# Optimization experiments

Measured on AMD Instinct MI355X. Metric: run time of the kernel, lower is better.

The kernel has to match this reference:

```python
import jax, jax.numpy as jnp
import numpy as np

V, Tb, D, H, L = 50257, 1024, 768, 12, 12
HS = D // H  # head size 64
DF = 4 * D   # MLP hidden 3072


def setup_inputs() -> dict:
    key = jax.random.key(0)
    ks = jax.random.split(key, 24)
    s = 0.02
    inp = {}
    inp['x'] = jax.random.randint(ks[0], (1, Tb), 0, V, dtype=jnp.int64)
    inp['wte'] = jax.random.normal(ks[1], (V, D), jnp.float32) * s
    inp['wpe'] = jax.random.normal(ks[2], (Tb, D), jnp.float32) * s
    # per-layer, per-head QKV linears, stacked: [L, H, D, HS]
    inp['Wq'] = jax.random.normal(ks[3], (L, H, D, HS), jnp.float32) * s
    inp['bq'] = jnp.zeros((L, H, HS), jnp.float32)
    inp['Wk'] = jax.random.normal(ks[4], (L, H, D, HS), jnp.float32) * s
    inp['bk'] = jnp.zeros((L, H, HS), jnp.float32)
    inp['Wv'] = jax.random.normal(ks[5], (L, H, D, HS), jnp.float32) * s
    inp['bv'] = jnp.zeros((L, H, HS), jnp.float32)
    inp['ln1_s'] = jnp.ones((L, D), jnp.float32)
    inp['ln1_b'] = jnp.zeros((L, D), jnp.float32)
    inp['W1'] = jax.random.normal(ks[6], (L, D, DF), jnp.float32) * s
    inp['b1'] = jnp.zeros((L, DF), jnp.float32)
    inp['W2'] = jax.random.normal(ks[7], (L, DF, D), jnp.float32) * s
    inp['b2'] = jnp.zeros((L, D), jnp.float32)
    inp['ln2_s'] = jnp.ones((L, D), jnp.float32)
    inp['ln2_b'] = jnp.zeros((L, D), jnp.float32)
    inp['lnf_s'] = jnp.ones((D,), jnp.float32)
    inp['lnf_b'] = jnp.zeros((D,), jnp.float32)
    inp['Wlm'] = jax.random.normal(ks[8], (D, V), jnp.float32) * s
    return inp


def _layernorm(x, scale, bias, eps=1e-5):
    mu = jnp.mean(x, axis=-1, keepdims=True)
    var = jnp.var(x, axis=-1, keepdims=True)
    return (x - mu) * jax.lax.rsqrt(var + eps) * scale + bias


def _gpt2_forward(x, wte, wpe, Wq, bq, Wk, bk, Wv, bv, ln1_s, ln1_b,
                  W1, b1, W2, b2, ln2_s, ln2_b, lnf_s, lnf_b, Wlm):
    B, T = x.shape
    h = wte[x] + wpe[jnp.arange(T)][None]  # [B, T, D]
    mask = jnp.tril(jnp.ones((T, T), jnp.bool_))
    for l in range(L):
        xn = _layernorm(h, ln1_s[l], ln1_b[l])
        # per-head linears, stacked -> [B, H, T, HS]
        q = jnp.einsum('btd,hde->bhte', xn, Wq[l]) + bq[l][None, :, None, :]
        k = jnp.einsum('btd,hde->bhte', xn, Wk[l]) + bk[l][None, :, None, :]
        v = jnp.einsum('btd,hde->bhte', xn, Wv[l]) + bv[l][None, :, None, :]
        # NOTE: original module does NOT scale scores by 1/sqrt(head_size)
        scores = jnp.einsum('bhte,bhse->bhts', q, k)
        scores = jnp.where(mask[None, None], scores, -jnp.inf)
        w = jax.nn.softmax(scores, axis=-1)
        attn = jnp.einsum('bhts,bhse->bhte', w, v)
        attn = attn.transpose(0, 2, 1, 3).reshape(B, T, H * HS)
        h = h + attn  # residual (no output projection in original)
        xn2 = _layernorm(h, ln2_s[l], ln2_b[l])
        mlp = jnp.einsum('btd,df->btf', xn2, W1[l]) + b1[l]
        mlp = jax.nn.gelu(mlp, approximate=False)  # nn.GELU default = exact
        mlp = jnp.einsum('btf,fd->btd', mlp, W2[l]) + b2[l]
        h = h + mlp
    h = _layernorm(h, lnf_s, lnf_b)
    logits = jnp.einsum('btd,dv->btv', h, Wlm)  # lm_head, no bias
    return logits


def reference(x, wte, wpe, Wq, bq, Wk, bk, Wv, bv, ln1_s, ln1_b,
              W1, b1, W2, b2, ln2_s, ln2_b, lnf_s, lnf_b, Wlm):
    return _gpt2_forward(x, wte, wpe, Wq, bq, Wk, bk, Wv, bv, ln1_s, ln1_b,
                         W1, b1, W2, b2, ln2_s, ln2_b, lnf_s, lnf_b, Wlm)
```

## Files before the change

### kernel.cpp

```cpp
#include <hip/hip_runtime.h>
#include <math.h>

#define TLEN 1024
#define DM   768
#define NH   12
#define HSZ  64
#define DF_  3072
#define NL   12
#define VC   50257
#define VCP  50304
#define NPAN (VCP/128)

typedef __attribute__((ext_vector_type(8))) short bf16x8;
typedef __attribute__((ext_vector_type(4))) float f32x4;

__device__ __forceinline__ float gelu_exact(float x){
  return 0.5f * x * (1.0f + erff(x * 0.70710678118654752f));
}
__device__ __forceinline__ short f2bf(float f){
  union { float f; unsigned u; } x; x.f = f;
  unsigned r = x.u + 0x7fffu + ((x.u >> 16) & 1u);
  return (short)(r >> 16);
}
__device__ __forceinline__ void gl16(const void* g, void* l){
  __builtin_amdgcn_global_load_lds(
      (const __attribute__((address_space(1))) unsigned int*)g,
      (__attribute__((address_space(3))) unsigned int*)l, 16, 0, 0);
}

__global__ __launch_bounds__(256) void embed_k(const int* __restrict__ x,
    const float* __restrict__ wte, const float* __restrict__ wpe,
    float* __restrict__ h)
{
  int i = blockIdx.x * 256 + threadIdx.x;
  int t = i / DM, d = i - t * DM;
  h[i] = wte[(size_t)x[t] * DM + d] + wpe[i];
}

__global__ __launch_bounds__(256) void ln_k(const float* __restrict__ in,
    const float* __restrict__ sc, const float* __restrict__ bi,
    short* __restrict__ out)
{
  int w = threadIdx.x >> 6, lane = threadIdx.x & 63;
  int row = blockIdx.x * 4 + w;
  const float* r = in + (size_t)row * DM;
  float v[12];
  float s = 0.f, s2 = 0.f;
  #pragma unroll
  for (int i = 0; i < 12; i++){
    float xv = r[lane + i * 64];
    v[i] = xv; s += xv; s2 += xv * xv;
  }
  #pragma unroll
  for (int off = 32; off; off >>= 1){
    s  += __shfl_xor(s,  off);
    s2 += __shfl_xor(s2, off);
  }
  float mu  = s * (1.0f / DM);
  float var = s2 * (1.0f / DM) - mu * mu;
  float rs  = rsqrtf(var + 1e-5f);
  short* o = out + (size_t)row * DM;
  #pragma unroll
  for (int i = 0; i < 12; i++){
    int c = lane + i * 64;
    o[c] = f2bf((v[i] - mu) * rs * sc[c] + bi[c]);
  }
}

__global__ __launch_bounds__(256) void tc_k(const float* __restrict__ in,
    short* __restrict__ out, int K, int N, int ntiles, int per_mat,
    size_t in_stride, size_t out_stride)
{
  __shared__ short sh[64][65];
  int b = blockIdx.x;
  int l = b / per_mat, r = b - l * per_mat;
  int nt = r % ntiles, kt = r / ntiles;
  const float* ip = in + (size_t)l * in_stride;
  short* op = out + (size_t)l * out_stride;
  int n0 = nt * 64, k0 = kt * 64;
  int tid = threadIdx.x;
  if ((N & 3) == 0){
    #pragma unroll
    for (int it = 0; it < 4; it++){
      int idx = it * 256 + tid;
      int k = idx >> 4, n4 = (idx & 15) * 4;
      float4 v = *(const float4*)(ip + (size_t)(k0 + k) * N + n0 + n4);
      sh[k][n4+0] = f2bf(v.x); sh[k][n4+1] = f2bf(v.y);
      sh[k][n4+2] = f2bf(v.z); sh[k][n4+3] = f2bf(v.w);
    }
  } else {
    #pragma unroll
    for (int it = 0; it < 16; it++){
      int idx = it * 256 + tid;
      int k = idx >> 6, n = idx & 63;
      float v = (n0 + n < N) ? ip[(size_t)(k0 + k) * N + n0 + n] : 0.f;
      sh[k][n] = f2bf(v);
    }
  }
  __syncthreads();
  #pragma unroll
  for (int it = 0; it < 2; it++){
    int n = it * 32 + (tid >> 3);
    int kc = (tid & 7) * 8;
    bf16x8 v;
    #pragma unroll
    for (int u = 0; u < 8; u++) v[u] = sh[kc + u][n];
    *(bf16x8*)(op + (size_t)(n0 + n) * K + k0 + kc) = v;
  }
}

__global__ __launch_bounds__(256) void tcqkv_k(const float* __restrict__ Wq,
    const float* __restrict__ Wk, const float* __restrict__ Wv,
    short* __restrict__ out)
{
  __shared__ short sh[64][65];
  int b = blockIdx.x;
  int l = b / 144; int r = b - l * 144;
  int h = r / 12, kt = r - h * 12;
  int tid = threadIdx.x;
  for (int p = 0; p < 3; p++){
    const float* ip = (p == 0 ? Wq : p == 1 ? Wk : Wv)
                      + ((size_t)(l * NH + h) * DM + kt * 64) * 64;
    if (p) __syncthreads();
    #pragma unroll
    for (int it = 0; it < 4; it++){
      int idx = it * 256 + tid;
      int k = idx >> 4, e4 = (idx & 15) * 4;
      float4 v = *(const float4*)(ip + (size_t)k * 64 + e4);
      sh[k][e4+0] = f2bf(v.x); sh[k][e4+1] = f2bf(v.y);
      sh[k][e4+2] = f2bf(v.z); sh[k][e4+3] = f2bf(v.w);
    }
    __syncthreads();
    short* op = out + (size_t)l * 2304 * DM + (size_t)(p * DM + h * 64) * DM;
    #pragma unroll
    for (int it = 0; it < 2; it++){
      int e = it * 32 + (tid >> 3);
      int kc = (tid & 7) * 8;
      bf16x8 v;
      #pragma unroll
      for (int u = 0; u < 8; u++) v[u] = sh[kc + u][e];
      *(bf16x8*)(op + (size_t)e * DM + kt * 64 + kc) = v;
    }
  }
}

template<int MODE, int FI, int FJ>
__global__ __launch_bounds__(256) void mg_k(
    const short* __restrict__ A, const short* __restrict__ Bt,
    const float* __restrict__ b0, const float* __restrict__ b1,
    const float* __restrict__ b2,
    void* __restrict__ C0, void* __restrict__ C1, void* __restrict__ C2)
{
  constexpr int LDA    = (MODE == 2) ? DF_ : DM;
  constexpr int BM     = FI * 32;
  constexpr int BN     = FJ * 32;
  constexpr int ABYTES = BM * 64 * 2;
  constexpr int BBYTES = BN * 64 * 2;
  __shared__ __align__(16) char lds[2 * (ABYTES + BBYTES)];

  int tid = threadIdx.x;
  int wid = tid >> 6, lane = tid & 63;
  int l15 = lane & 15, l4 = lane >> 4;
  int wr = wid >> 1, wc = wid & 1;

  int m0, n0;
  if (MODE == 3){
    int xcd = blockIdx.x & 7, slot = blockIdx.x >> 3;
    int nb = xcd + 8 * (slot >> 3);
    if (nb >= NPAN) return;
    m0 = (slot & 7) * BM;
    n0 = nb * BN;
  } else {
    m0 = blockIdx.x * BM;
    n0 = blockIdx.y * BN;
  }
  int kbeg = (MODE == 2) ? blockIdx.z * (DF_ / 4) : 0;
  int nk   = ((MODE == 2) ? DF_ / 4 : LDA) / 64;

  f32x4 acc[FI][FJ] = {};
  int wbase = (tid & ~63) * 16;

  auto stage = [&](int k0, int b){
    char* ab = lds + b * ABYTES;
    char* bb = lds + 2 * ABYTES + b * BBYTES;
    #pragma unroll
    for (int ia = 0; ia < FI; ia++){
      int d = ia * 256 + tid;
      int row = d >> 3, gs = (d & 7) ^ (row & 7);
      gl16(A + (size_t)(m0 + row) * LDA + k0 + gs * 8, ab + ia * 4096 + wbase);
    }
    #pragma unroll
    for (int ib = 0; ib < FJ; ib++){
      int d = ib * 256 + tid;
      int row = d >> 3, gs = (d & 7) ^ (row & 7);
      gl16(Bt + (size_t)(n0 + row) * LDA + k0 + gs * 8, bb + ib * 4096 + wbase);
    }
  };

  stage(kbeg, 0);
  int cur = 0;
  for (int t = 0; t < nk; ++t){
    int k0 = kbeg + t * 64;
    if (t + 1 < nk){
      stage(k0 + 64, cur ^ 1);
      if constexpr (FI + FJ == 4) asm volatile("s_waitcnt vmcnt(4)" ::: "memory");
      else                        asm volatile("s_waitcnt vmcnt(8)" ::: "memory");
    } else {
      asm volatile("s_waitcnt vmcnt(0)" ::: "memory");
    }
    __builtin_amdgcn_s_barrier();
    __builtin_amdgcn_sched_barrier(0);

    char* ab = lds + cur * ABYTES;
    char* bb = lds + 2 * ABYTES + cur * BBYTES;
    #pragma unroll
    for (int kk = 0; kk < 2; kk++){
      bf16x8 af[FI], bfr[FJ];
      #pragma unroll
      for (int i = 0; i < FI; i++){
        int row = wr * (FI * 16) + i * 16 + l15;
        af[i] = *(const bf16x8*)(ab + row * 128 + (((kk * 4 + l4) ^ (row & 7)) * 16));
      }
      #pragma unroll
      for (int j = 0; j < FJ; j++){
        int row = wc * (FJ * 16) + j * 16 + l15;
        bfr[j] = *(const bf16x8*)(bb + row * 128 + (((kk * 4 + l4) ^ (row & 7)) * 16));
      }
      #pragma unroll
      for (int i = 0; i < FI; i++)
        #pragma unroll
        for (int j = 0; j < FJ; j++)
          acc[i][j] = __builtin_amdgcn_mfma_f32_16x16x32_bf16(af[i], bfr[j], acc[i][j], 0, 0, 0);
    }
    __builtin_amdgcn_sched_barrier(0);
    __builtin_amdgcn_s_barrier();
    cur ^= 1;
  }

  #pragma unroll
  for (int i = 0; i < FI; i++){
    int rowb = m0 + wr * (FI * 16) + i * 16 + l4 * 4;
    #pragma unroll
    for (int j = 0; j < FJ; j++){
      int col = n0 + wc * (FJ * 16) + j * 16 + l15;
      if (MODE == 0){
        int p = col / DM, within = col - p * DM;
        const float* bp = (p == 0) ? b0 : (p == 1) ? b1 : b2;
        float bb2 = bp[within];
        int hd = within >> 6, e = within & 63;
        if (p < 2){
          short* dst = (short*)((p == 0) ? C0 : C1);
          #pragma unroll
          for (int r = 0; r < 4; r++)
            dst[((size_t)hd * TLEN + rowb + r) * 64 + e] = f2bf(acc[i][j][r] + bb2);
        } else {
          short4 pk;
          pk.x = f2bf(acc[i][j][0] + bb2); pk.y = f2bf(acc[i][j][1] + bb2);
          pk.z = f2bf(acc[i][j][2] + bb2); pk.w = f2bf(acc[i][j][3] + bb2);
          *(short4*)((short*)C2 + ((size_t)hd * 64 + e) * TLEN + rowb) = pk;
        }
      } else if (MODE == 1){
        #pragma unroll
        for (int r = 0; r < 4; r++)
          ((short*)C0)[(size_t)(rowb + r) * DF_ + col] =
              f2bf(gelu_exact(acc[i][j][r] + b0[col]));
      } else if (MODE == 2){
        #pragma unroll
        for (int r = 0; r < 4; r++){
          float add = acc[i][j][r] + (blockIdx.z == 0 ? b0[col] : 0.f);
          atomicAdd((float*)C0 + (size_t)(rowb + r) * DM + col, add);
        }
      } else {
        if (col < VC){
          #pragma unroll
          for (int r = 0; r < 4; r++)
            ((float*)C0)[(size_t)(rowb + r) * VC + col] = acc[i][j][r];
        }
      }
    }
  }
}

__global__ __launch_bounds__(256) void attn_k(const short* __restrict__ q,
    const short* __restrict__ k, const short* __restrict__ vt,
    float* __restrict__ h)
{
  __shared__ short P_lds[4][16][72];
  int tid = threadIdx.x;
  int wid = tid >> 6, lane = tid & 63;
  int l15 = lane & 15, l4 = lane >> 4;
  int head = blockIdx.x >> 4, qt = blockIdx.x & 15;
  int qb = qt * 64 + wid * 16;

  const short* qh = q  + (size_t)head * TLEN * 64;
  const short* kh = k  + (size_t)head * TLEN * 64;
  const short* vh = vt + (size_t)head * 64 * TLEN;

  bf16x8 qf[2];
  qf[0] = *(const bf16x8*)(qh + (size_t)(qb + l15) * 64 + l4 * 8);
  qf[1] = *(const bf16x8*)(qh + (size_t)(qb + l15) * 64 + 32 + l4 * 8);

  f32x4 O[4] = {};
  float mrow[4] = {-3e38f, -3e38f, -3e38f, -3e38f};
  float lrow[4] = {0.f, 0.f, 0.f, 0.f};

  for (int kv0 = 0; kv0 <= qb + 15; kv0 += 64){
    f32x4 S[4] = {};
    #pragma unroll
    for (int kk = 0; kk < 2; kk++){
      #pragma unroll
      for (int j = 0; j < 4; j++){
        bf16x8 kf = *(const bf16x8*)(kh + (size_t)(kv0 + j*16 + l15) * 64
                                     + kk*32 + l4*8);
        S[j] = __builtin_amdgcn_mfma_f32_16x16x32_bf16(qf[kk], kf, S[j], 0, 0, 0);
      }
    }
    if (kv0 + 63 > qb){
      #pragma unroll
      for (int j = 0; j < 4; j++){
        int kvc = kv0 + j*16 + l15;
        #pragma unroll
        for (int r = 0; r < 4; r++)
          if (kvc > qb + l4*4 + r) S[j][r] = -3e38f;
      }
    }
    #pragma unroll
    for (int r = 0; r < 4; r++){
      float mx = fmaxf(fmaxf(S[0][r], S[1][r]), fmaxf(S[2][r], S[3][r]));
      #pragma unroll
      for (int off = 1; off < 16; off <<= 1) mx = fmaxf(mx, __shfl_xor(mx, off));
      float mn = fmaxf(mrow[r], mx);
      float corr = __expf(mrow[r] - mn);
      mrow[r] = mn;
      float sm = 0.f;
      #pragma unroll
      for (int j = 0; j < 4; j++){
        float p = __expf(S[j][r] - mn);
        S[j][r] = p; sm += p;
      }
      #pragma unroll
      for (int off = 1; off < 16; off <<= 1) sm += __shfl_xor(sm, off);
      lrow[r] = lrow[r] * corr + sm;
      #pragma unroll
      for (int j = 0; j < 4; j++) O[j][r] *= corr;
    }
    #pragma unroll
    for (int j = 0; j < 4; j++)
      #pragma unroll
      for (int r = 0; r < 4; r++)
        P_lds[wid][l4*4 + r][j*16 + l15] = f2bf(S[j][r]);
    #pragma unroll
    for (int kk = 0; kk < 2; kk++){
      bf16x8 pa = *(const bf16x8*)(&P_lds[wid][l15][kk*32 + l4*8]);
      #pragma unroll
      for (int jd = 0; jd < 4; jd++){
        bf16x8 vf = *(const bf16x8*)(vh + (size_t)(jd*16 + l15) * TLEN
                                     + kv0 + kk*32 + l4*8);
        O[jd] = __builtin_amdgcn_mfma_f32_16x16x32_bf16(pa, vf, O[jd], 0, 0, 0);
      }
    }
  }

  #pragma unroll
  for (int r = 0; r < 4; r++){
    float inv = 1.0f / lrow[r];
    int t = qb + l4*4 + r;
    #pragma unroll
    for (int jd = 0; jd < 4; jd++){
      int d = head * 64 + jd*16 + l15;
      h[(size_t)t * DM + d] += O[jd][r] * inv;
    }
  }
}

extern "C" void kernel_launch(void* const* d_in, const int* in_sizes, int n_in,
                              void* d_out, int out_size, void* d_ws, size_t ws_size,
                              hipStream_t stream)
{
  const int*   x    = (const int*)  d_in[0];
  const float* wte  = (const float*)d_in[1];
  const float* wpe  = (const float*)d_in[2];
  const float* Wq   = (const float*)d_in[3];
  const float* bq   = (const float*)d_in[4];
  const float* Wk   = (const float*)d_in[5];
  const float* bk   = (const float*)d_in[6];
  const float* Wv   = (const float*)d_in[7];
  const float* bv   = (const float*)d_in[8];
  const float* ln1s = (const float*)d_in[9];
  const float* ln1b = (const float*)d_in[10];
  const float* W1   = (const float*)d_in[11];
  const float* b1   = (const float*)d_in[12];
  const float* W2   = (const float*)d_in[13];
  const float* b2   = (const float*)d_in[14];
  const float* ln2s = (const float*)d_in[15];
  const float* ln2b = (const float*)d_in[16];
  const float* lnfs = (const float*)d_in[17];
  const float* lnfb = (const float*)d_in[18];
  const float* Wlm  = (const float*)d_in[19];
  float* out = (float*)d_out;

  const size_t SZ_QKVT = (size_t)NL * 2304 * DM * 2;
  const size_t SZ_W1T  = (size_t)NL * DF_ * DM * 2;
  const size_t SZ_W2T  = (size_t)NL * DM * DF_ * 2;
  const size_t SZ_WLMT = (size_t)VCP * DM * 2;
  const size_t SZ_H    = (size_t)TLEN * DM * 4;
  const size_t SZ_BF   = (size_t)TLEN * DM * 2;

  char* ws = (char*)d_ws;
  short* wqkvT = (short*)ws;  ws += SZ_QKVT;
  short* w1T   = (short*)ws;  ws += SZ_W1T;
  short* w2T   = (short*)ws;  ws += SZ_W2T;
  short* wlmT  = (short*)ws;  ws += SZ_WLMT;
  float* h     = (float*)ws;  ws += SZ_H;
  short* qb    = (short*)ws;  ws += SZ_BF;
  short* kb    = (short*)ws;  ws += SZ_BF;
  short* vtb   = (short*)ws;  ws += SZ_BF;
  short* xnb   = (short*)ws;  ws += SZ_BF;
  short* mhb   = (short*)ws;

  tcqkv_k<<<NL*NH*12, 256, 0, stream>>>(Wq, Wk, Wv, wqkvT);
  tc_k<<<NL*48*12, 256, 0, stream>>>(W1, w1T, DM, DF_, 48, 576,
                                     (size_t)DM*DF_, (size_t)DM*DF_);
  tc_k<<<NL*12*48, 256, 0, stream>>>(W2, w2T, DF_, DM, 12, 576,
                                     (size_t)DM*DF_, (size_t)DM*DF_);
  tc_k<<<786*12, 256, 0, stream>>>(Wlm, wlmT, DM, VC, 786, 786*12, 0, 0);

  embed_k<<<TLEN*DM/256, 256, 0, stream>>>(x, wte, wpe, h);

  for (int l = 0; l < NL; ++l){
    ln_k<<<TLEN/4, 256, 0, stream>>>(h, ln1s + l*DM, ln1b + l*DM, xnb);
    mg_k<0,2,2><<<dim3(16,36), 256, 0, stream>>>(xnb, wqkvT + (size_t)l*2304*DM,
        bq + l*DM, bk + l*DM, bv + l*DM, qb, kb, vtb);
    attn_k<<<NH*16, 256, 0, stream>>>(qb, kb, vtb, h);
    ln_k<<<TLEN/4, 256, 0, stream>>>(h, ln2s + l*DM, ln2b + l*DM, xnb);
    mg_k<1,2,2><<<dim3(16,48), 256, 0, stream>>>(xnb, w1T + (size_t)l*DF_*DM,
        b1 + l*DF_, nullptr, nullptr, mhb, nullptr, nullptr);
    mg_k<2,2,2><<<dim3(16,12,4), 256, 0, stream>>>(mhb, w2T + (size_t)l*DM*DF_,
        b2 + l*DM, nullptr, nullptr, h, nullptr, nullptr);
  }

  ln_k<<<TLEN/4, 256, 0, stream>>>(h, lnfs, lnfb, xnb);
  mg_k<3,4,4><<<3200, 256, 0, stream>>>(xnb, wlmT,
      nullptr, nullptr, nullptr, out, nullptr, nullptr);
}
```

Measured before the change: 1.337 ms.

## Replace atomic split-K with two partial buffers reduced in fused residual+LayerNorm

The MLP down-projection moves from a 4-way split-K with float atomicAdd into h to a 2-way split writing plain partial buffers (p0 reuses the q buffer, p1 is new workspace). A new kernel adds both partials, the bias and the residual, then applies the next layer's LN1 (or the final LN), which removes a separate LN launch per layer. Embedding is also fused with the first LayerNorm. This drops atomic traffic and a launch and a pass over h per layer, but halves the down-projection's grid parallelism and adds partial-buffer writes and reads.

```diff
diff --git a/kernel.cpp b/kernel.cpp
--- a/kernel.cpp
+++ b/kernel.cpp
@@ -28,13 +28,34 @@
       (__attribute__((address_space(3))) unsigned int*)l, 16, 0, 0);
 }
 
-__global__ __launch_bounds__(256) void embed_k(const int* __restrict__ x,
+__global__ __launch_bounds__(256) void embedln_k(const int* __restrict__ x,
     const float* __restrict__ wte, const float* __restrict__ wpe,
-    float* __restrict__ h)
-{
-  int i = blockIdx.x * 256 + threadIdx.x;
-  int t = i / DM, d = i - t * DM;
-  h[i] = wte[(size_t)x[t] * DM + d] + wpe[i];
+    const float* __restrict__ sc, const float* __restrict__ bi,
+    float* __restrict__ h, short* __restrict__ out)
+{
+  int w = threadIdx.x >> 6, lane = threadIdx.x & 63;
+  int t = blockIdx.x * 4 + w;
+  int tok = x[t];
+  size_t off = (size_t)t * DM;
+  float v[12];
+  float s = 0.f, s2 = 0.f;
+  #pragma unroll
+  for (int i = 0; i < 12; i++){
+    int c = lane + i * 64;
+    float xv = wte[(size_t)tok * DM + c] + wpe[off + c];
+    h[off + c] = xv;
+    v[i] = xv; s += xv; s2 += xv * xv;
+  }
+  #pragma unroll
+  for (int o = 32; o; o >>= 1){ s += __shfl_xor(s, o); s2 += __shfl_xor(s2, o); }
+  float mu = s * (1.0f / DM);
+  float var = s2 * (1.0f / DM) - mu * mu;
+  float rs = rsqrtf(var + 1e-5f);
+  #pragma unroll
+  for (int i = 0; i < 12; i++){
+    int c = lane + i * 64;
+    out[off + c] = f2bf((v[i] - mu) * rs * sc[c] + bi[c]);
+  }
 }
 
 __global__ __launch_bounds__(256) void ln_k(const float* __restrict__ in,
@@ -52,10 +73,7 @@
     v[i] = xv; s += xv; s2 += xv * xv;
   }
   #pragma unroll
-  for (int off = 32; off; off >>= 1){
-    s  += __shfl_xor(s,  off);
-    s2 += __shfl_xor(s2, off);
-  }
+  for (int o = 32; o; o >>= 1){ s += __shfl_xor(s, o); s2 += __shfl_xor(s2, o); }
   float mu  = s * (1.0f / DM);
   float var = s2 * (1.0f / DM) - mu * mu;
   float rs  = rsqrtf(var + 1e-5f);
@@ -64,6 +82,36 @@
   for (int i = 0; i < 12; i++){
     int c = lane + i * 64;
     o[c] = f2bf((v[i] - mu) * rs * sc[c] + bi[c]);
+  }
+}
+
+__global__ __launch_bounds__(256) void redln_k(float* __restrict__ h,
+    const float* __restrict__ p0, const float* __restrict__ p1,
+    const float* __restrict__ bias,
+    const float* __restrict__ sc, const float* __restrict__ bi,
+    short* __restrict__ out)
+{
+  int w = threadIdx.x >> 6, lane = threadIdx.x & 63;
+  int row = blockIdx.x * 4 + w;
+  size_t off = (size_t)row * DM;
+  float v[12];
+  float s = 0.f, s2 = 0.f;
+  #pragma unroll
+  for (int i = 0; i < 12; i++){
+    int c = lane + i * 64;
+    float xv = h[off + c] + p0[off + c] + p1[off + c] + bias[c];
+    h[off + c] = xv;
+    v[i] = xv; s += xv; s2 += xv * xv;
+  }
+  #pragma unroll
+  for (int o = 32; o; o >>= 1){ s += __shfl_xor(s, o); s2 += __shfl_xor(s2, o); }
+  float mu  = s * (1.0f / DM);
+  float var = s2 * (1.0f / DM) - mu * mu;
+  float rs  = rsqrtf(var + 1e-5f);
+  #pragma unroll
+  for (int i = 0; i < 12; i++){
+    int c = lane + i * 64;
+    out[off + c] = f2bf((v[i] - mu) * rs * sc[c] + bi[c]);
   }
 }
 
@@ -174,8 +222,8 @@
     m0 = blockIdx.x * BM;
     n0 = blockIdx.y * BN;
   }
-  int kbeg = (MODE == 2) ? blockIdx.z * (DF_ / 4) : 0;
-  int nk   = ((MODE == 2) ? DF_ / 4 : LDA) / 64;
+  int kbeg = (MODE == 2) ? blockIdx.z * (DF_ / 2) : 0;
+  int nk   = ((MODE == 2) ? DF_ / 2 : LDA) / 64;
 
   f32x4 acc[FI][FJ] = {};
   int wbase = (tid & ~63) * 16;
@@ -265,11 +313,10 @@
           ((short*)C0)[(size_t)(rowb + r) * DF_ + col] =
               f2bf(gelu_exact(acc[i][j][r] + b0[col]));
       } else if (MODE == 2){
+        float* dst = (float*)((blockIdx.z == 0) ? C0 : C1);
         #pragma unroll
-        for (int r = 0; r < 4; r++){
-          float add = acc[i][j][r] + (blockIdx.z == 0 ? b0[col] : 0.f);
-          atomicAdd((float*)C0 + (size_t)(rowb + r) * DM + col, add);
-        }
+        for (int r = 0; r < 4; r++)
+          dst[(size_t)(rowb + r) * DM + col] = acc[i][j][r];
       } else {
         if (col < VC){
           #pragma unroll
@@ -416,7 +463,9 @@
   short* kb    = (short*)ws;  ws += SZ_BF;
   short* vtb   = (short*)ws;  ws += SZ_BF;
   short* xnb   = (short*)ws;  ws += SZ_BF;
-  short* mhb   = (short*)ws;
+  short* mhb   = (short*)ws;  ws += (size_t)TLEN * DF_ * 2;
+  float* p1    = (float*)ws;
+  float* p0    = (float*)qb;
 
   tcqkv_k<<<NL*NH*12, 256, 0, stream>>>(Wq, Wk, Wv, wqkvT);
   tc_k<<<NL*48*12, 256, 0, stream>>>(W1, w1T, DM, DF_, 48, 576,
@@ -425,21 +474,22 @@
                                      (size_t)DM*DF_, (size_t)DM*DF_);
   tc_k<<<786*12, 256, 0, stream>>>(Wlm, wlmT, DM, VC, 786, 786*12, 0, 0);
 
-  embed_k<<<TLEN*DM/256, 256, 0, stream>>>(x, wte, wpe, h);
+  embedln_k<<<TLEN/4, 256, 0, stream>>>(x, wte, wpe, ln1s, ln1b, h, xnb);
 
   for (int l = 0; l < NL; ++l){
-    ln_k<<<TLEN/4, 256, 0, stream>>>(h, ln1s + l*DM, ln1b + l*DM, xnb);
     mg_k<0,2,2><<<dim3(16,36), 256, 0, stream>>>(xnb, wqkvT + (size_t)l*2304*DM,
         bq + l*DM, bk + l*DM, bv + l*DM, qb, kb, vtb);
     attn_k<<<NH*16, 256, 0, stream>>>(qb, kb, vtb, h);
     ln_k<<<TLEN/4, 256, 0, stream>>>(h, ln2s + l*DM, ln2b + l*DM, xnb);
     mg_k<1,2,2><<<dim3(16,48), 256, 0, stream>>>(xnb, w1T + (size_t)l*DF_*DM,
         b1 + l*DF_, nullptr, nullptr, mhb, nullptr, nullptr);
-    mg_k<2,2,2><<<dim3(16,12,4), 256, 0, stream>>>(mhb, w2T + (size_t)l*DM*DF_,
-        b2 + l*DM, nullptr, nullptr, h, nullptr, nullptr);
-  }
-
-  ln_k<<<TLEN/4, 256, 0, stream>>>(h, lnfs, lnfb, xnb);
+    mg_k<2,2,2><<<dim3(16,12,2), 256, 0, stream>>>(mhb, w2T + (size_t)l*DM*DF_,
+        nullptr, nullptr, nullptr, p0, p1, nullptr);
+    const float* nsc = (l < NL-1) ? ln1s + (l+1)*DM : lnfs;
+    const float* nbi = (l < NL-1) ? ln1b + (l+1)*DM : lnfb;
+    redln_k<<<TLEN/4, 256, 0, stream>>>(h, p0, p1, b2 + l*DM, nsc, nbi, xnb);
+  }
+
   mg_k<3,4,4><<<3200, 256, 0, stream>>>(xnb, wlmT,
       nullptr, nullptr, nullptr, out, nullptr, nullptr);
 }
```

Measured after the change: 1.316 ms. About the same (-1.6%).
